# Performance work log

Measured on AMD Instinct MI355X. Metric: run time of the kernel, lower is better.

Reference implementation:

```python
import jax, jax.numpy as jnp
import numpy as np
import math

MODEL_DIM = 4096
NUM_EXPERTS = 64
NUM_TOKENS = 8192
CAPACITY_FACTOR = 1.0
MIN_CAPACITY = 4


def setup_inputs() -> dict:
    key = jax.random.key(0)
    k1, k2, k3 = jax.random.split(key, 3)
    x = jax.random.normal(k1, (NUM_TOKENS, MODEL_DIM), dtype=jnp.float32)
    wg_weight = jax.random.normal(k2, (NUM_EXPERTS, MODEL_DIM), dtype=jnp.float32) * (1.0 / math.sqrt(MODEL_DIM))
    uniform_noise = jax.random.uniform(k3, (NUM_TOKENS, NUM_EXPERTS), dtype=jnp.float32)
    return {"x": x, "wg_weight": wg_weight, "uniform_noise": uniform_noise}


def reference(x, wg_weight, uniform_noise):
    # gate projection in fp32 (torch module forces .float())
    logits = jnp.einsum('sd,ed->se', x.astype(jnp.float32), wg_weight.astype(jnp.float32))
    gates = jax.nn.softmax(logits, axis=1)  # [s, e]
    s, e = gates.shape
    capacity = max(math.ceil(s / e * CAPACITY_FACTOR), MIN_CAPACITY)  # static: 128

    indices1_s = jnp.argmax(gates, axis=1)                      # [s]
    mask1 = jax.nn.one_hot(indices1_s, e, dtype=jnp.int32)      # [s, e]
    exp_counts = jnp.sum(mask1, axis=0)                         # [e]

    # load-balancing aux loss
    me = jnp.mean(gates, axis=0)
    ce = jnp.mean(mask1.astype(jnp.float32), axis=0)
    l_aux = jnp.sum(me * ce) * e

    # random capacity selection: per-expert top-`capacity` tokens by uniform noise
    mask1_rand = mask1.astype(jnp.float32) * uniform_noise      # [s, e]
    _, top_idx = jax.lax.top_k(mask1_rand.T, capacity)          # [e, capacity] token ids
    sel = jnp.zeros((s, e), jnp.int32).at[top_idx, jnp.arange(e)[:, None]].set(1)
    new_mask1 = mask1 * sel                                     # [s, e]

    # capacity-slot assignment via cumsum
    locations1 = jnp.cumsum(new_mask1, axis=0) - 1              # [s, e]
    locations1_s = jnp.sum(locations1 * new_mask1, axis=1)      # [s]

    gates_masked = gates * new_mask1.astype(jnp.float32)        # [s, e]
    locations1_sc = jax.nn.one_hot(locations1_s, capacity, dtype=jnp.float32)  # [s, c]
    combine_weights = jnp.einsum('se,sc->sec', gates_masked, locations1_sc)     # [s, e, c]
    dispatch_mask = combine_weights.astype(bool)
    return l_aux, combine_weights, dispatch_mask, exp_counts
```

## Files before the change

### kernel.cpp

```cpp
#include <hip/hip_runtime.h>

#define S    8192
#define Dm   4096
#define E    64
#define CAP  128
#define CCH  32
#define KC   (Dm/CCH)
#define KSUB 16
#define XSTR 260
#define WSTR 68

#define CW_OFF 1
#define DM_OFF (1 + (size_t)S*E*CAP)
#define EC_OFF (1 + 2*(size_t)S*E*CAP)

__global__ __launch_bounds__(256, 4)
void k1_partial(const float* __restrict__ x, const float* __restrict__ wg,
                float* __restrict__ part) {
    __shared__ float xs[KSUB][XSTR];
    __shared__ float wsh[KSUB][WSTR];
    const int tb  = blockIdx.x >> 5;
    const int c   = blockIdx.x & 31;
    const int tid = threadIdx.x;
    const int tt  = tid & 31;
    const int ee  = tid >> 5;
    const int k0  = c * KC;

    float acc[64];
    #pragma unroll
    for (int i = 0; i < 64; i++) acc[i] = 0.f;

    const int xr = tid >> 2;
    const int xc = tid & 3;
    const int we = tid >> 2;
    const int wk = (tid & 3) * 4;

    for (int su = 0; su < KC / KSUB; su++) {
        const int ks0 = k0 + su * KSUB;
        #pragma unroll
        for (int i = 0; i < 4; i++) {
            const int row = i * 64 + xr;
            const float4 v = *(const float4*)(x + (size_t)(tb*256 + row) * Dm + ks0 + xc*4);
            xs[xc*4+0][row] = v.x;
            xs[xc*4+1][row] = v.y;
            xs[xc*4+2][row] = v.z;
            xs[xc*4+3][row] = v.w;
        }
        {
            const float4 v = *(const float4*)(wg + (size_t)we * Dm + ks0 + wk);
            wsh[wk+0][we] = v.x; wsh[wk+1][we] = v.y;
            wsh[wk+2][we] = v.z; wsh[wk+3][we] = v.w;
        }
        __syncthreads();
        #pragma unroll 4
        for (int kk = 0; kk < KSUB; kk++) {
            const float4 a0 = *(const float4*)&xs[kk][tt*4];
            const float4 a1 = *(const float4*)&xs[kk][128 + tt*4];
            const float4 w0 = *(const float4*)&wsh[kk][ee*8];
            const float4 w1 = *(const float4*)&wsh[kk][ee*8+4];
            const float av[8] = {a0.x,a0.y,a0.z,a0.w,a1.x,a1.y,a1.z,a1.w};
            const float wv[8] = {w0.x,w0.y,w0.z,w0.w,w1.x,w1.y,w1.z,w1.w};
            #pragma unroll
            for (int t = 0; t < 8; t++)
                #pragma unroll
                for (int e = 0; e < 8; e++)
                    acc[t*8+e] = fmaf(av[t], wv[e], acc[t*8+e]);
        }
        __syncthreads();
    }
    #pragma unroll
    for (int t = 0; t < 8; t++) {
        const int token = (t < 4) ? (tt*4 + t) : (128 + tt*4 + (t - 4));
        float* dst = part + ((size_t)c * S + tb*256 + token) * E + ee*8;
        *(float4*)(dst)     = make_float4(acc[t*8+0], acc[t*8+1], acc[t*8+2], acc[t*8+3]);
        *(float4*)(dst + 4) = make_float4(acc[t*8+4], acc[t*8+5], acc[t*8+6], acc[t*8+7]);
    }
}

__global__ __launch_bounds__(256, 1)
void k1b_softmax(const float* __restrict__ part, float* __restrict__ gate_val,
                 int* __restrict__ idx1, int* __restrict__ counts,
                 float* __restrict__ me_sum) {
    const int tid = threadIdx.x, wv = tid >> 6, ln = tid & 63;
    const int token = blockIdx.x * 4 + wv;
    float p = 0.f;
    #pragma unroll
    for (int c = 0; c < CCH; c++) p += part[((size_t)c * S + token) * E + ln];
    float v = p; int i = ln;
    #pragma unroll
    for (int off = 1; off < 64; off <<= 1) {
        float ov = __shfl_xor(v, off, 64);
        int   oi = __shfl_xor(i, off, 64);
        if (ov > v || (ov == v && oi < i)) { v = ov; i = oi; }
    }
    float g = __expf(p - v);
    float ssum = g;
    #pragma unroll
    for (int off = 1; off < 64; off <<= 1) ssum += __shfl_xor(ssum, off, 64);
    const float gate = g / ssum;
    __shared__ float gs[4][64];
    gs[wv][ln] = gate;
    __syncthreads();
    if (tid < 64)
        atomicAdd(&me_sum[tid], gs[0][tid] + gs[1][tid] + gs[2][tid] + gs[3][tid]);
    if (ln == 0) {
        gate_val[token] = 1.0f / ssum;
        idx1[token] = i;
        atomicAdd(&counts[i], 1);
    }
}

__device__ __forceinline__ int block_reduce_sum(int v, int* tmp4, int tid) {
    #pragma unroll
    for (int off = 1; off < 64; off <<= 1) v += __shfl_xor(v, off, 64);
    __syncthreads();
    if ((tid & 63) == 0) tmp4[tid >> 6] = v;
    __syncthreads();
    return tmp4[0] + tmp4[1] + tmp4[2] + tmp4[3];
}

__device__ __forceinline__ int block_scan_incl(int val, int* a, int* b, int tid, int* total) {
    __syncthreads();
    a[tid] = val;
    __syncthreads();
    int* src = a; int* dst = b;
    #pragma unroll
    for (int off = 1; off < 256; off <<= 1) {
        int v = src[tid];
        if (tid >= off) v += src[tid - off];
        dst[tid] = v;
        __syncthreads();
        int* t = src; src = dst; dst = t;
    }
    *total = src[255];
    return src[tid];
}

__global__ __launch_bounds__(256, 1)
void k2_select(const int* __restrict__ idx1, const float* __restrict__ gate_val,
               const float* __restrict__ noise, const int* __restrict__ counts,
               const float* __restrict__ me_sum, float* __restrict__ out) {
    const int e = blockIdx.x;
    const int tid = threadIdx.x;
    __shared__ int idx_s[S];
    __shared__ unsigned short l_tok[S];
    __shared__ float l_ns[S];
    __shared__ int sa[256], sb[256];
    __shared__ int tmp4[4];

    for (int i = tid; i < S; i += 256) idx_s[i] = idx1[i];
    __syncthreads();

    int cnt = 0;
    #pragma unroll
    for (int j4 = 0; j4 < 8; j4++) {
        const int4 q = *(const int4*)&idx_s[tid * 32 + j4 * 4];
        cnt += (q.x == e) + (q.y == e) + (q.z == e) + (q.w == e);
    }
    int total_n;
    int incl = block_scan_incl(cnt, sa, sb, tid, &total_n);
    int pos = incl - cnt;
    const int n = total_n;
    #pragma unroll
    for (int j4 = 0; j4 < 8; j4++) {
        const int4 q = *(const int4*)&idx_s[tid * 32 + j4 * 4];
        const int qv[4] = {q.x, q.y, q.z, q.w};
        #pragma unroll
        for (int u = 0; u < 4; u++) {
            const int s = tid * 32 + j4 * 4 + u;
            if (qv[u] == e) {
                l_tok[pos] = (unsigned short)s;
                l_ns[pos]  = noise[(size_t)s * E + e];
                pos++;
            }
        }
    }
    __syncthreads();

    if (tid == 0) out[EC_OFF + e] = (float)n;

    unsigned int V = 0u;
    if (n > CAP) {
        unsigned int lo = 0u, hi = 0x3F800000u;
        while (hi - lo > 1u) {
            const unsigned int mid = (lo + hi) >> 1;
            int c = 0;
            for (int i2 = tid; i2 < n; i2 += 256)
                c += (__float_as_uint(l_ns[i2]) >= mid);
            const int cge = block_reduce_sum(c, tmp4, tid);
            if (cge >= CAP) lo = mid; else hi = mid;
        }
        V = lo;
    }

    const int m = (n + 255) >> 8;
    const int i_begin = min(n, tid * m);
    const int i_end   = min(n, i_begin + m);
    int gt_l = 0, eq_l = 0;
    for (int i2 = i_begin; i2 < i_end; i2++) {
        const unsigned int b = __float_as_uint(l_ns[i2]);
        gt_l += (b > V); eq_l += (b == V);
    }
    int tot_gt, tot_eq;
    const int incl_gt = block_scan_incl(gt_l, sa, sb, tid, &tot_gt);
    (void)incl_gt;
    const int incl_eq = block_scan_incl(eq_l, sa, sb, tid, &tot_eq);
    const int eq_excl = incl_eq - eq_l;
    const int take_eq = CAP - tot_gt;
    const int sel_l = gt_l + max(0, min(eq_l, take_eq - eq_excl));
    int tot_sel;
    const int incl_sel = block_scan_incl(sel_l, sa, sb, tid, &tot_sel);
    int slot = incl_sel - sel_l;
    int eq_seen = eq_excl;
    for (int i2 = i_begin; i2 < i_end; i2++) {
        const unsigned int b = __float_as_uint(l_ns[i2]);
        bool sel;
        if (b > V) sel = true;
        else if (b == V) { sel = (eq_seen < take_eq); eq_seen++; }
        else sel = false;
        if (sel) {
            const int tok = l_tok[i2];
            const float g = gate_val[tok];
            const size_t off = (size_t)tok * (E * CAP) + (size_t)e * CAP + slot;
            out[CW_OFF + off] = g;
            out[DM_OFF + off] = 1.0f;
            slot++;
        }
    }

    if (e == 0 && tid < 64) {
        float la = (me_sum[tid] / (float)S) * ((float)counts[tid] / (float)S);
        #pragma unroll
        for (int off = 1; off < 64; off <<= 1) la += __shfl_xor(la, off, 64);
        if (tid == 0) out[0] = la * (float)E;
    }
}

extern "C" void kernel_launch(void* const* d_in, const int* in_sizes, int n_in,
                              void* d_out, int out_size, void* d_ws, size_t ws_size,
                              hipStream_t stream) {
    const float* x     = (const float*)d_in[0];
    const float* wg    = (const float*)d_in[1];
    const float* noise = (const float*)d_in[2];
    float* out = (float*)d_out;
    float* ws  = (float*)d_ws;

    float* gate_val = ws;
    int*   idx1     = (int*)(ws + 8192);
    int*   counts   = (int*)(ws + 16384);
    float* me_sum   = ws + 16448;
    float* part     = ws + 16512;

    hipMemsetAsync(counts, 0, 128 * sizeof(int), stream);
    hipMemsetAsync(out, 0, (size_t)out_size * sizeof(float), stream);
    k1_partial  <<<dim3(1024), dim3(256), 0, stream>>>(x, wg, part);
    k1b_softmax <<<dim3(S/4),  dim3(256), 0, stream>>>(part, gate_val, idx1, counts, me_sum);
    k2_select   <<<dim3(E),    dim3(256), 0, stream>>>(idx1, gate_val, noise, counts, me_sum, out);
}
```

Baseline: 711.6 us.

## Fuse output zeroing into gate GEMM kernel and replace me_sum atomics with partials

Drops the full-output hipMemsetAsync (about 1 GB of zeros) and has the k1_partial blocks write the zeros with nontemporal stores inside their K loop. The goal is to overlap the memory-bound zeroing with the compute-bound gate projection. k1b_softmax now handles 16 tokens per block and writes per-block me partials instead of doing atomicAdd into me_sum. k2_select then reduces those partials serially. This removes the atomics and a separate memset pass, but adds store pressure inside the GEMM loop and a 512-iteration serial reduction for the aux loss.

```diff
diff --git a/kernel.cpp b/kernel.cpp
--- a/kernel.cpp
+++ b/kernel.cpp
@@ -13,10 +13,16 @@
 #define CW_OFF 1
 #define DM_OFF (1 + (size_t)S*E*CAP)
 #define EC_OFF (1 + 2*(size_t)S*E*CAP)
+#define OUT_FLOATS (1 + 2*(size_t)S*E*CAP + E)
+#define ZERO_MAIN  (2*(size_t)S*E*CAP)
+#define ZPB        (ZERO_MAIN/1024)
+#define K1B_BLOCKS 512
+
+typedef float f32x4 __attribute__((ext_vector_type(4)));
 
 __global__ __launch_bounds__(256, 4)
 void k1_partial(const float* __restrict__ x, const float* __restrict__ wg,
-                float* __restrict__ part) {
+                float* __restrict__ part, float* __restrict__ out) {
     __shared__ float xs[KSUB][XSTR];
     __shared__ float wsh[KSUB][WSTR];
     const int tb  = blockIdx.x >> 5;
@@ -26,6 +32,11 @@
     const int ee  = tid >> 5;
     const int k0  = c * KC;
 
+    if (blockIdx.x == 0 && tid < 65)
+        __builtin_nontemporal_store(0.f, out + ZERO_MAIN + tid);
+    f32x4* const zbase = (f32x4*)(out + (size_t)blockIdx.x * ZPB);
+    const f32x4 zf4 = {0.f, 0.f, 0.f, 0.f};
+
     float acc[64];
     #pragma unroll
     for (int i = 0; i < 64; i++) acc[i] = 0.f;
@@ -50,6 +61,11 @@
             const float4 v = *(const float4*)(wg + (size_t)we * Dm + ks0 + wk);
             wsh[wk+0][we] = v.x; wsh[wk+1][we] = v.y;
             wsh[wk+2][we] = v.z; wsh[wk+3][we] = v.w;
+        }
+        #pragma unroll
+        for (int z = 0; z < 16; z++) {
+            const int zi = su * 16 + z;
+            __builtin_nontemporal_store(zf4, zbase + (size_t)zi * 256 + tid);
         }
         __syncthreads();
         #pragma unroll 4
@@ -80,34 +96,38 @@
 __global__ __launch_bounds__(256, 1)
 void k1b_softmax(const float* __restrict__ part, float* __restrict__ gate_val,
                  int* __restrict__ idx1, int* __restrict__ counts,
-                 float* __restrict__ me_sum) {
+                 float* __restrict__ me_part) {
     const int tid = threadIdx.x, wv = tid >> 6, ln = tid & 63;
-    const int token = blockIdx.x * 4 + wv;
-    float p = 0.f;
-    #pragma unroll
-    for (int c = 0; c < CCH; c++) p += part[((size_t)c * S + token) * E + ln];
-    float v = p; int i = ln;
-    #pragma unroll
-    for (int off = 1; off < 64; off <<= 1) {
-        float ov = __shfl_xor(v, off, 64);
-        int   oi = __shfl_xor(i, off, 64);
-        if (ov > v || (ov == v && oi < i)) { v = ov; i = oi; }
-    }
-    float g = __expf(p - v);
-    float ssum = g;
-    #pragma unroll
-    for (int off = 1; off < 64; off <<= 1) ssum += __shfl_xor(ssum, off, 64);
-    const float gate = g / ssum;
+    float me_loc = 0.f;
+    #pragma unroll
+    for (int t = 0; t < 4; t++) {
+        const int token = blockIdx.x * 16 + wv * 4 + t;
+        float p = 0.f;
+        #pragma unroll
+        for (int c = 0; c < CCH; c++) p += part[((size_t)c * S + token) * E + ln];
+        float v = p; int i = ln;
+        #pragma unroll
+        for (int off = 1; off < 64; off <<= 1) {
+            float ov = __shfl_xor(v, off, 64);
+            int   oi = __shfl_xor(i, off, 64);
+            if (ov > v || (ov == v && oi < i)) { v = ov; i = oi; }
+        }
+        float g = __expf(p - v);
+        float ssum = g;
+        #pragma unroll
+        for (int off = 1; off < 64; off <<= 1) ssum += __shfl_xor(ssum, off, 64);
+        me_loc += g / ssum;
+        if (ln == 0) {
+            gate_val[token] = 1.0f / ssum;
+            idx1[token] = i;
+            atomicAdd(&counts[i], 1);
+        }
+    }
     __shared__ float gs[4][64];
-    gs[wv][ln] = gate;
+    gs[wv][ln] = me_loc;
     __syncthreads();
     if (tid < 64)
-        atomicAdd(&me_sum[tid], gs[0][tid] + gs[1][tid] + gs[2][tid] + gs[3][tid]);
-    if (ln == 0) {
-        gate_val[token] = 1.0f / ssum;
-        idx1[token] = i;
-        atomicAdd(&counts[i], 1);
-    }
+        me_part[(size_t)blockIdx.x * 64 + tid] = gs[0][tid] + gs[1][tid] + gs[2][tid] + gs[3][tid];
 }
 
 __device__ __forceinline__ int block_reduce_sum(int v, int* tmp4, int tid) {
@@ -139,7 +159,7 @@
 __global__ __launch_bounds__(256, 1)
 void k2_select(const int* __restrict__ idx1, const float* __restrict__ gate_val,
                const float* __restrict__ noise, const int* __restrict__ counts,
-               const float* __restrict__ me_sum, float* __restrict__ out) {
+               const float* __restrict__ me_part, float* __restrict__ out) {
     const int e = blockIdx.x;
     const int tid = threadIdx.x;
     __shared__ int idx_s[S];
@@ -229,7 +249,9 @@
     }
 
     if (e == 0 && tid < 64) {
-        float la = (me_sum[tid] / (float)S) * ((float)counts[tid] / (float)S);
+        float ms = 0.f;
+        for (int b2 = 0; b2 < K1B_BLOCKS; b2++) ms += me_part[(size_t)b2 * 64 + tid];
+        float la = (ms / (float)S) * ((float)counts[tid] / (float)S);
         #pragma unroll
         for (int off = 1; off < 64; off <<= 1) la += __shfl_xor(la, off, 64);
         if (tid == 0) out[0] = la * (float)E;
@@ -248,12 +270,11 @@
     float* gate_val = ws;
     int*   idx1     = (int*)(ws + 8192);
     int*   counts   = (int*)(ws + 16384);
-    float* me_sum   = ws + 16448;
-    float* part     = ws + 16512;
-
-    hipMemsetAsync(counts, 0, 128 * sizeof(int), stream);
-    hipMemsetAsync(out, 0, (size_t)out_size * sizeof(float), stream);
-    k1_partial  <<<dim3(1024), dim3(256), 0, stream>>>(x, wg, part);
-    k1b_softmax <<<dim3(S/4),  dim3(256), 0, stream>>>(part, gate_val, idx1, counts, me_sum);
-    k2_select   <<<dim3(E),    dim3(256), 0, stream>>>(idx1, gate_val, noise, counts, me_sum, out);
-}
+    float* me_part  = ws + 16448;
+    float* part     = ws + 49216;
+
+    (void)hipMemsetAsync(counts, 0, 64 * sizeof(int), stream);
+    k1_partial  <<<dim3(1024),       dim3(256), 0, stream>>>(x, wg, part, out);
+    k1b_softmax <<<dim3(K1B_BLOCKS), dim3(256), 0, stream>>>(part, gate_val, idx1, counts, me_part);
+    k2_select   <<<dim3(E),          dim3(256), 0, stream>>>(idx1, gate_val, noise, counts, me_part, out);
+}
```

After: 737.0 us. +3.6%, slower.
